# Optimization experiments

Hardware: AMD Instinct MI355X
Metric: run time of the kernel (lower is better)

## Reference

```python
import jax, jax.numpy as jnp
import numpy as np
from jax import lax

IN_CH = 256
OUT_CH = 256
INTER = IN_CH // 2
KERNEL = 3


def setup_inputs() -> dict:
    key = jax.random.key(0)
    ks = jax.random.split(key, 6)
    B, C, H, W = 8, IN_CH, 128, 128
    x = jax.random.normal(ks[0], (B, C, H, W), dtype=jnp.float32)
    s = 1.0 / np.sqrt(C)
    Wq = jax.random.normal(ks[1], (INTER, C), dtype=jnp.float32) * s
    Wk = jax.random.normal(ks[2], (INTER, C), dtype=jnp.float32) * s
    Wv = jax.random.normal(ks[3], (INTER, C), dtype=jnp.float32) * s
    w1d = jax.random.normal(ks[4], (KERNEL,), dtype=jnp.float32) * (1.0 / np.sqrt(KERNEL))
    Wc = jax.random.normal(ks[5], (OUT_CH, INTER, 3, 3), dtype=jnp.float32) * (1.0 / np.sqrt(INTER * 9))
    return {"x": x, "Wq": Wq, "Wk": Wk, "Wv": Wv, "w1d": w1d, "Wc": Wc}


def reference(x, Wq, Wk, Wv, w1d, Wc):
    B, C, H, W = x.shape
    inter = Wq.shape[0]
    Hs, Ws = H // 4, W // 4  # 1x1 conv, stride 4, pad 0 == spatial subsample
    xs = x[:, :, ::4, ::4]  # [B, C, Hs, Ws]
    q = jnp.einsum('oc,bchw->bohw', Wq, xs).reshape(B, inter, Hs * Ws)  # [B, inter, N]
    k = jnp.einsum('oc,bchw->bohw', Wk, xs).reshape(B, inter, Hs * Ws)
    v = jnp.einsum('oc,bchw->bohw', Wv, xs).reshape(B, inter, Hs * Ws)
    # gate = softmax(Q^T K) over last dim, shape [B, N, N]
    scores = jnp.einsum('bcn,bcm->bnm', q, k)
    gate = jax.nn.softmax(scores, axis=-1)
    # gated value: [B, inter, N] -> [B, inter, Hs, Ws]
    gv = jnp.einsum('bnm,bcm->bcn', gate, v).reshape(B, inter, Hs, Ws)
    # ECA channel gating: global avg pool -> conv1d over channel dim -> sigmoid
    ca = gv.mean(axis=(2, 3))  # [B, inter]
    ca = lax.conv_general_dilated(
        ca[:, None, :],                     # [B, 1, inter]
        w1d[None, None, :],                 # [1, 1, K]
        window_strides=(1,), padding=[((KERNEL - 1) // 2,) * 2],
        dimension_numbers=('NCH', 'OIH', 'NCH'))
    ca = jax.nn.sigmoid(ca)[:, 0, :, None, None]  # [B, inter, 1, 1]
    out = gv * ca
    out = lax.conv_general_dilated(
        out, Wc, window_strides=(1, 1), padding='SAME',
        dimension_numbers=('NCHW', 'OIHW', 'NCHW'))
    return out, gate, ca
```

## Files before the change

### kernel.cpp

```cpp
#include <hip/hip_runtime.h>
#include <math.h>

#define B_   8
#define C_   256
#define CI_  128
#define N_   1024
#define HW_  32
#define CO_  256

typedef __bf16 v8bf __attribute__((ext_vector_type(8)));
typedef float  f32x4 __attribute__((ext_vector_type(4)));
typedef unsigned short ushort_t;

__device__ __forceinline__ unsigned short f2bf_rne(float f) {
    unsigned int u = __float_as_uint(f);
    unsigned int r = u + 0x7FFF + ((u >> 16) & 1);
    return (unsigned short)(r >> 16);
}
__device__ __forceinline__ float bf2f(unsigned short h) {
    return __uint_as_float(((unsigned int)h) << 16);
}
__device__ __forceinline__ v8bf ld8(const ushort_t* p) {
    return *(const v8bf*)p;
}

__global__ __launch_bounds__(256) void prep_w_kernel(
    const float* __restrict__ Wc,
    const float* __restrict__ Wq, const float* __restrict__ Wk,
    const float* __restrict__ Wv,
    ushort_t* __restrict__ Whi, ushort_t* __restrict__ Wlo,
    ushort_t* __restrict__ Wp_hi, ushort_t* __restrict__ Wp_lo)
{
    if (blockIdx.x < 1152) {
        int idx = blockIdx.x * 256 + threadIdx.x;
        int o = idx / 1152;
        int r = idx - o * 1152;
        int ci = r / 9;
        int tap = r - ci * 9;
        float v = Wc[idx];
        unsigned short h = f2bf_rne(v);
        unsigned short l = f2bf_rne(v - bf2f(h));
        int didx = o * 1152 + tap * 128 + ci;
        Whi[didx] = h; Wlo[didx] = l;
    } else {
        int j = (blockIdx.x - 1152) * 256 + threadIdx.x;
        int o = j >> 8, c = j & 255;
        float v = (o < 128) ? Wq[o * 256 + c]
                : (o < 256) ? Wk[(o - 128) * 256 + c]
                            : Wv[(o - 256) * 256 + c];
        unsigned short h = f2bf_rne(v);
        unsigned short l = f2bf_rne(v - bf2f(h));
        Wp_hi[j] = h; Wp_lo[j] = l;
    }
}

__global__ __launch_bounds__(256) void prep_x_kernel(
    const float* __restrict__ x,
    ushort_t* __restrict__ xs_hi, ushort_t* __restrict__ xs_lo)
{
    __shared__ ushort_t lh[32 * 264];
    __shared__ ushort_t ll[32 * 264];
    const int h = blockIdx.x, b = blockIdx.y;
    const int tid = threadIdx.x;
    const int w = tid & 31, cg = tid >> 5;
    for (int c0 = 0; c0 < 256; c0 += 8) {
        int c = c0 + cg;
        float v = x[((size_t)(b * C_ + c) * 128 + h * 4) * 128 + w * 4];
        unsigned short hi = f2bf_rne(v);
        unsigned short lo = f2bf_rne(v - bf2f(hi));
        lh[w * 264 + c] = hi;
        ll[w * 264 + c] = lo;
    }
    __syncthreads();
    const int ww = tid >> 3, cs = tid & 7;
    size_t dst = ((size_t)(b * N_) + h * 32 + ww) * 256 + cs * 32;
    #pragma unroll
    for (int t = 0; t < 4; ++t) {
        *(uint4*)&xs_hi[dst + t * 8] = *(uint4*)&lh[ww * 264 + cs * 32 + t * 8];
        *(uint4*)&xs_lo[dst + t * 8] = *(uint4*)&ll[ww * 264 + cs * 32 + t * 8];
    }
}

__global__ __launch_bounds__(256) void proj_mfma_kernel(
    const ushort_t* __restrict__ Wp_hi, const ushort_t* __restrict__ Wp_lo,
    const ushort_t* __restrict__ xs_hi, const ushort_t* __restrict__ xs_lo,
    ushort_t* __restrict__ qt_hi, ushort_t* __restrict__ qt_lo,
    ushort_t* __restrict__ kt_hi, ushort_t* __restrict__ kt_lo,
    ushort_t* __restrict__ vB_hi, ushort_t* __restrict__ vB_lo)
{
    const int n0 = blockIdx.x * 64;
    const int o0 = blockIdx.y * 64;
    const int b  = blockIdx.z;
    const int tid = threadIdx.x;
    const int l = tid & 63, wv = tid >> 6;
    const int wy = wv >> 1, wx = wv & 1;
    const int ln = l & 15, quad = l >> 4;

    f32x4 acc[2][2];
    #pragma unroll
    for (int i = 0; i < 2; ++i)
        #pragma unroll
        for (int j = 0; j < 2; ++j) acc[i][j] = (f32x4){0.f,0.f,0.f,0.f};

    const ushort_t* Ah_p[2]; const ushort_t* Al_p[2];
    const ushort_t* Bh_p[2]; const ushort_t* Bl_p[2];
    #pragma unroll
    for (int i = 0; i < 2; ++i) {
        size_t off = (size_t)(o0 + wy * 32 + i * 16 + ln) * 256 + quad * 8;
        Ah_p[i] = Wp_hi + off; Al_p[i] = Wp_lo + off;
    }
    #pragma unroll
    for (int j = 0; j < 2; ++j) {
        size_t off = ((size_t)(b * N_) + n0 + wx * 32 + j * 16 + ln) * 256 + quad * 8;
        Bh_p[j] = xs_hi + off; Bl_p[j] = xs_lo + off;
    }

    #pragma unroll 4
    for (int k0 = 0; k0 < 256; k0 += 32) {
        v8bf Ah[2], Al[2], Bh[2], Bl[2];
        #pragma unroll
        for (int i = 0; i < 2; ++i) { Ah[i] = ld8(Ah_p[i] + k0); Al[i] = ld8(Al_p[i] + k0); }
        #pragma unroll
        for (int j = 0; j < 2; ++j) { Bh[j] = ld8(Bh_p[j] + k0); Bl[j] = ld8(Bl_p[j] + k0); }
        #pragma unroll
        for (int i = 0; i < 2; ++i)
            #pragma unroll
            for (int j = 0; j < 2; ++j) {
                acc[i][j] = __builtin_amdgcn_mfma_f32_16x16x32_bf16(Ah[i], Bh[j], acc[i][j], 0, 0, 0);
                acc[i][j] = __builtin_amdgcn_mfma_f32_16x16x32_bf16(Ah[i], Bl[j], acc[i][j], 0, 0, 0);
                acc[i][j] = __builtin_amdgcn_mfma_f32_16x16x32_bf16(Al[i], Bh[j], acc[i][j], 0, 0, 0);
            }
    }

    if (o0 < 256) {
        ushort_t* th = (o0 < 128) ? qt_hi : kt_hi;
        ushort_t* tl = (o0 < 128) ? qt_lo : kt_lo;
        const int ob = o0 & 127;
        #pragma unroll
        for (int i = 0; i < 2; ++i)
            #pragma unroll
            for (int j = 0; j < 2; ++j) {
                int oo = ob + wy * 32 + i * 16 + quad * 4;
                int n  = n0 + wx * 32 + j * 16 + ln;
                unsigned int h01 = 0, h23 = 0, l01 = 0, l23 = 0;
                #pragma unroll
                for (int r = 0; r < 4; ++r) {
                    float f = acc[i][j][r];
                    unsigned short hh = f2bf_rne(f);
                    unsigned short lo = f2bf_rne(f - bf2f(hh));
                    if (r < 2) { h01 |= ((unsigned)hh) << (16 * r); l01 |= ((unsigned)lo) << (16 * r); }
                    else       { h23 |= ((unsigned)hh) << (16 * (r - 2)); l23 |= ((unsigned)lo) << (16 * (r - 2)); }
                }
                size_t off = ((size_t)(b * N_) + n) * 128 + oo;
                *(uint2*)&th[off] = make_uint2(h01, h23);
                *(uint2*)&tl[off] = make_uint2(l01, l23);
            }
    } else {
        #pragma unroll
        for (int i = 0; i < 2; ++i)
            #pragma unroll
            for (int j = 0; j < 2; ++j)
                #pragma unroll
                for (int r = 0; r < 4; ++r) {
                    int c = (o0 - 256) + wy * 32 + i * 16 + quad * 4 + r;
                    int m = n0 + wx * 32 + j * 16 + ln;
                    float f = acc[i][j][r];
                    unsigned short hh = f2bf_rne(f);
                    unsigned short lo = f2bf_rne(f - bf2f(hh));
                    size_t off = (((size_t)b * 32 + (m >> 5)) * 128 + c) * 32 + (m & 31);
                    vB_hi[off] = hh; vB_lo[off] = lo;
                }
    }
}

__global__ __launch_bounds__(256, 1) void attn_fused_kernel(
    const ushort_t* __restrict__ qt_hi, const ushort_t* __restrict__ qt_lo,
    const ushort_t* __restrict__ kt_hi, const ushort_t* __restrict__ kt_lo,
    const ushort_t* __restrict__ vB_hi, const ushort_t* __restrict__ vB_lo,
    float* __restrict__ gate, float* __restrict__ gv)
{
    __shared__ __align__(16) char gsm[65536];
    __shared__ float redA[4][32];
    __shared__ float redB[4][32];

    const int n0 = blockIdx.x * 32;
    const int b  = blockIdx.y;
    const int tid = threadIdx.x;
    const int l = tid & 63, w = tid >> 6;
    const int ln = l & 15, quad = l >> 4;
    const int Mw = w * 256;

    const ushort_t* qb_h = qt_hi + ((size_t)(b * N_) + n0) * 128;
    const ushort_t* qb_l = qt_lo + ((size_t)(b * N_) + n0) * 128;
    const ushort_t* kb_h = kt_hi + (size_t)(b * N_) * 128;
    const ushort_t* kb_l = kt_lo + (size_t)(b * N_) * 128;

    f32x4 acc[2][16];
    #pragma unroll
    for (int nt = 0; nt < 2; ++nt)
        #pragma unroll
        for (int mt = 0; mt < 16; ++mt) acc[nt][mt] = (f32x4){0.f,0.f,0.f,0.f};

    #pragma unroll
    for (int c0 = 0; c0 < 128; c0 += 32) {
        v8bf Ah[2], Al[2];
        #pragma unroll
        for (int nt = 0; nt < 2; ++nt) {
            size_t aoff = (size_t)(nt * 16 + ln) * 128 + c0 + quad * 8;
            Ah[nt] = ld8(qb_h + aoff); Al[nt] = ld8(qb_l + aoff);
        }
        #pragma unroll
        for (int mt = 0; mt < 16; ++mt) {
            size_t boff = (size_t)(Mw + mt * 16 + ln) * 128 + c0 + quad * 8;
            v8bf Bh = ld8(kb_h + boff);
            v8bf Bl = ld8(kb_l + boff);
            #pragma unroll
            for (int nt = 0; nt < 2; ++nt) {
                acc[nt][mt] = __builtin_amdgcn_mfma_f32_16x16x32_bf16(Ah[nt], Bh, acc[nt][mt], 0, 0, 0);
                acc[nt][mt] = __builtin_amdgcn_mfma_f32_16x16x32_bf16(Ah[nt], Bl, acc[nt][mt], 0, 0, 0);
                acc[nt][mt] = __builtin_amdgcn_mfma_f32_16x16x32_bf16(Al[nt], Bh, acc[nt][mt], 0, 0, 0);
            }
        }
    }

    float rmax[2][4];
    #pragma unroll
    for (int nt = 0; nt < 2; ++nt)
        #pragma unroll
        for (int r = 0; r < 4; ++r) {
            float m = acc[nt][0][r];
            #pragma unroll
            for (int mt = 1; mt < 16; ++mt) m = fmaxf(m, acc[nt][mt][r]);
            rmax[nt][r] = m;
        }
    #pragma unroll
    for (int nt = 0; nt < 2; ++nt)
        #pragma unroll
        for (int r = 0; r < 4; ++r) {
            float m = rmax[nt][r];
            #pragma unroll
            for (int xm = 1; xm <= 8; xm <<= 1) m = fmaxf(m, __shfl_xor(m, xm, 64));
            rmax[nt][r] = m;
        }
    if (ln == 0) {
        #pragma unroll
        for (int nt = 0; nt < 2; ++nt)
            #pragma unroll
            for (int r = 0; r < 4; ++r)
                redA[w][nt * 16 + quad * 4 + r] = rmax[nt][r];
    }
    __syncthreads();
    #pragma unroll
    for (int nt = 0; nt < 2; ++nt)
        #pragma unroll
        for (int r = 0; r < 4; ++r) {
            int row = nt * 16 + quad * 4 + r;
            rmax[nt][r] = fmaxf(fmaxf(redA[0][row], redA[1][row]),
                                fmaxf(redA[2][row], redA[3][row]));
        }

    float rsum[2][4];
    #pragma unroll
    for (int nt = 0; nt < 2; ++nt)
        #pragma unroll
        for (int r = 0; r < 4; ++r) {
            float s = 0.f;
            #pragma unroll
            for (int mt = 0; mt < 16; ++mt) {
                float e = __expf(acc[nt][mt][r] - rmax[nt][r]);
                acc[nt][mt][r] = e;
                s += e;
            }
            rsum[nt][r] = s;
        }
    #pragma unroll
    for (int nt = 0; nt < 2; ++nt)
        #pragma unroll
        for (int r = 0; r < 4; ++r) {
            float s = rsum[nt][r];
            #pragma unroll
            for (int xm = 1; xm <= 8; xm <<= 1) s += __shfl_xor(s, xm, 64);
            rsum[nt][r] = s;
        }
    if (ln == 0) {
        #pragma unroll
        for (int nt = 0; nt < 2; ++nt)
            #pragma unroll
            for (int r = 0; r < 4; ++r)
                redB[w][nt * 16 + quad * 4 + r] = rsum[nt][r];
    }
    __syncthreads();
    #pragma unroll
    for (int nt = 0; nt < 2; ++nt)
        #pragma unroll
        for (int r = 0; r < 4; ++r) {
            int row = nt * 16 + quad * 4 + r;
            float inv = 1.0f / (redB[0][row] + redB[1][row] + redB[2][row] + redB[3][row]);
            #pragma unroll
            for (int mt = 0; mt < 16; ++mt) acc[nt][mt][r] *= inv;
        }

    float* grow = gate + (size_t)b * N_ * N_;
    #pragma unroll
    for (int nt = 0; nt < 2; ++nt)
        #pragma unroll
        for (int r = 0; r < 4; ++r) {
            int n  = n0 + nt * 16 + quad * 4 + r;
            int nl = nt * 16 + quad * 4 + r;
            #pragma unroll
            for (int mt = 0; mt < 16; ++mt) {
                int m = Mw + mt * 16 + ln;
                float v = acc[nt][mt][r];
                grow[(size_t)n * N_ + m] = v;
                int chunk = m >> 3;
                int addr = nl * 2048 + (((chunk ^ (nl & 7))) << 4) + ((m & 7) << 1);
                *(ushort_t*)&gsm[addr] = f2bf_rne(v);
            }
        }
    __syncthreads();

    const ushort_t* vb_h = vB_hi + (size_t)b * CI_ * N_;
    const ushort_t* vb_l = vB_lo + (size_t)b * CI_ * N_;

    f32x4 acc2[2][2];
    #pragma unroll
    for (int ct = 0; ct < 2; ++ct)
        #pragma unroll
        for (int nt = 0; nt < 2; ++nt) acc2[ct][nt] = (f32x4){0.f,0.f,0.f,0.f};

    #pragma unroll 4
    for (int m0 = 0; m0 < 1024; m0 += 32) {
        v8bf Bg[2];
        #pragma unroll
        for (int nt = 0; nt < 2; ++nt) {
            int nl = nt * 16 + ln;
            int chunk = (m0 >> 3) + quad;
            Bg[nt] = *(const v8bf*)&gsm[nl * 2048 + (((chunk ^ (nl & 7))) << 4)];
        }
        #pragma unroll
        for (int ct = 0; ct < 2; ++ct) {
            int c = w * 32 + ct * 16 + ln;
            size_t aoff = (((size_t)(m0 >> 5)) * 128 + c) * 32 + quad * 8;
            v8bf Avh = ld8(vb_h + aoff);
            v8bf Avl = ld8(vb_l + aoff);
            #pragma unroll
            for (int nt = 0; nt < 2; ++nt) {
                acc2[ct][nt] = __builtin_amdgcn_mfma_f32_16x16x32_bf16(Avh, Bg[nt], acc2[ct][nt], 0, 0, 0);
                acc2[ct][nt] = __builtin_amdgcn_mfma_f32_16x16x32_bf16(Avl, Bg[nt], acc2[ct][nt], 0, 0, 0);
            }
        }
    }

    #pragma unroll
    for (int ct = 0; ct < 2; ++ct)
        #pragma unroll
        for (int nt = 0; nt < 2; ++nt)
            #pragma unroll
            for (int r = 0; r < 4; ++r) {
                int c = w * 32 + ct * 16 + quad * 4 + r;
                int n = n0 + nt * 16 + ln;
                gv[(size_t)(b * CI_ + c) * N_ + n] = acc2[ct][nt][r];
            }
}

__global__ __launch_bounds__(256) void mean_kernel(
    const float* __restrict__ gv, float* __restrict__ meanb)
{
    const int i = blockIdx.x, b = blockIdx.y;
    const int tid = threadIdx.x;
    const int wid = tid >> 6, lane = tid & 63;
    __shared__ float red[4];
    const float* base = gv + (size_t)(b * CI_ + i) * N_;
    float4 v = ((const float4*)base)[tid];
    float s = v.x + v.y + v.z + v.w;
    #pragma unroll
    for (int off = 32; off; off >>= 1) s += __shfl_xor(s, off, 64);
    if (lane == 0) red[wid] = s;
    __syncthreads();
    if (tid == 0)
        meanb[b * CI_ + i] = (red[0] + red[1] + red[2] + red[3]) * (1.0f / 1024.0f);
}

__global__ __launch_bounds__(1024) void ca_kernel(
    const float* __restrict__ meanb, const float* __restrict__ w1d,
    float* __restrict__ ca)
{
    const int t = threadIdx.x;
    const int i = t & 127;
    float left  = (i > 0)   ? meanb[t - 1] : 0.0f;
    float mid   = meanb[t];
    float right = (i < 127) ? meanb[t + 1] : 0.0f;
    float val = w1d[0] * left + w1d[1] * mid + w1d[2] * right;
    ca[t] = 1.0f / (1.0f + __expf(-val));
}

#define BHI 0
#define BLO 17408
#define AHI 34816
#define ALO 43008
__global__ __launch_bounds__(256) void conv_mfma_kernel(
    const float* __restrict__ gv, const float* __restrict__ ca,
    const ushort_t* __restrict__ Whi, const ushort_t* __restrict__ Wlo,
    float* __restrict__ out)
{
    __shared__ char smem[51200];
    const int b   = blockIdx.z;
    const int h0  = blockIdx.y * 2;
    const int o0  = blockIdx.x * 64;
    const int tid = threadIdx.x;
    const int l   = tid & 63;
    const int wv  = tid >> 6;
    const int wy  = wv >> 1;
    const int wx  = wv & 1;
    const int ln  = l & 15;
    const int quad = l >> 4;

    f32x4 acc[2][2];
    #pragma unroll
    for (int i = 0; i < 2; ++i)
        #pragma unroll
        for (int j = 0; j < 2; ++j)
            acc[i][j] = (f32x4){0.f, 0.f, 0.f, 0.f};

    for (int half = 0; half < 2; ++half) {
        __syncthreads();
        for (int u = tid; u < 136 * 16; u += 256) {
            int p   = u >> 4;
            int ciq = u & 15;
            int hrel = p / 34;
            int c    = p - hrel * 34;
            int gr = h0 + hrel - 1;
            int gc = c - 1;
            bool ok = ((unsigned)gr < 32u) && ((unsigned)gc < 32u);
            int cib = half * 64 + ciq * 4;
            unsigned int hx = 0, hy = 0, lx = 0, ly = 0;
            #pragma unroll
            for (int t = 0; t < 4; ++t) {
                float v = 0.0f;
                if (ok)
                    v = gv[(size_t)(b * CI_ + cib + t) * N_ + gr * 32 + gc]
                        * ca[b * CI_ + cib + t];
                unsigned short h = f2bf_rne(v);
                unsigned short lo = f2bf_rne(v - bf2f(h));
                if (t < 2) { hx |= ((unsigned)h) << (16 * t); lx |= ((unsigned)lo) << (16 * t); }
                else       { hy |= ((unsigned)h) << (16 * (t - 2)); ly |= ((unsigned)lo) << (16 * (t - 2)); }
            }
            int addr = p * 128 + (((ciq >> 1) ^ (p & 7)) << 4) + ((ciq & 1) << 3);
            *(uint2*)&smem[BHI + addr] = make_uint2(hx, hy);
            *(uint2*)&smem[BLO + addr] = make_uint2(lx, ly);
        }
        for (int tap = 0; tap < 9; ++tap) {
            __syncthreads();
            #pragma unroll
            for (int it = 0; it < 2; ++it) {
                int row = it * 32 + (tid >> 3);
                int s   = tid & 7;
                int csrc = s ^ (row & 7);
                size_t gsrc = (size_t)(o0 + row) * 1152 + tap * 128 + half * 64 + csrc * 8;
                int la = row * 128 + s * 16;
                *(uint4*)&smem[AHI + la] = *(const uint4*)&Whi[gsrc];
                *(uint4*)&smem[ALO + la] = *(const uint4*)&Wlo[gsrc];
            }
            __syncthreads();
            const int dy = tap / 3, dx = tap - dy * 3;
            const int pbase = (wx + dy) * 34 + dx;
            #pragma unroll
            for (int cc = 0; cc < 2; ++cc) {
                v8bf Bh[2], Bl[2], Ah[2], Al[2];
                #pragma unroll
                for (int j = 0; j < 2; ++j) {
                    int p = pbase + j * 16 + ln;
                    int ch = cc * 4 + quad;
                    int addr = p * 128 + ((ch ^ (p & 7)) << 4);
                    Bh[j] = *(const v8bf*)&smem[BHI + addr];
                    Bl[j] = *(const v8bf*)&smem[BLO + addr];
                }
                #pragma unroll
                for (int i = 0; i < 2; ++i) {
                    int o = wy * 32 + i * 16 + ln;
                    int ch = cc * 4 + quad;
                    int addr = o * 128 + ((ch ^ (o & 7)) << 4);
                    Ah[i] = *(const v8bf*)&smem[AHI + addr];
                    Al[i] = *(const v8bf*)&smem[ALO + addr];
                }
                #pragma unroll
                for (int i = 0; i < 2; ++i)
                    #pragma unroll
                    for (int j = 0; j < 2; ++j) {
                        acc[i][j] = __builtin_amdgcn_mfma_f32_16x16x32_bf16(Ah[i], Bh[j], acc[i][j], 0, 0, 0);
                        acc[i][j] = __builtin_amdgcn_mfma_f32_16x16x32_bf16(Ah[i], Bl[j], acc[i][j], 0, 0, 0);
                        acc[i][j] = __builtin_amdgcn_mfma_f32_16x16x32_bf16(Al[i], Bh[j], acc[i][j], 0, 0, 0);
                    }
            }
        }
    }

    const int h = h0 + wx;
    #pragma unroll
    for (int i = 0; i < 2; ++i)
        #pragma unroll
        for (int j = 0; j < 2; ++j)
            #pragma unroll
            for (int r = 0; r < 4; ++r) {
                int o = o0 + wy * 32 + i * 16 + quad * 4 + r;
                int w = j * 16 + ln;
                out[(size_t)(b * CO_ + o) * N_ + h * 32 + w] = acc[i][j][r];
            }
}

extern "C" void kernel_launch(void* const* d_in, const int* in_sizes, int n_in,
                              void* d_out, int out_size, void* d_ws, size_t ws_size,
                              hipStream_t stream) {
    const float* x   = (const float*)d_in[0];
    const float* Wq  = (const float*)d_in[1];
    const float* Wk  = (const float*)d_in[2];
    const float* Wv  = (const float*)d_in[3];
    const float* w1d = (const float*)d_in[4];
    const float* Wc  = (const float*)d_in[5];

    float* out  = (float*)d_out;
    float* gate = out + 2097152;
    float* ca   = gate + 8388608;

    float*    gv      = (float*)d_ws;
    float*    meanb   = gv + 1048576;
    ushort_t* Whi     = (ushort_t*)(meanb + 1024);
    ushort_t* Wlo     = Whi + 294912;
    ushort_t* Wp_hi   = Wlo + 294912;
    ushort_t* Wp_lo   = Wp_hi + 98304;
    ushort_t* xs_hi   = Wp_lo + 98304;
    ushort_t* xs_lo   = xs_hi + 2097152;
    ushort_t* qt_hi   = xs_lo + 2097152;
    ushort_t* qt_lo   = qt_hi + 1048576;
    ushort_t* kt_hi   = qt_lo + 1048576;
    ushort_t* kt_lo   = kt_hi + 1048576;
    ushort_t* vB_hi   = kt_lo + 1048576;
    ushort_t* vB_lo   = vB_hi + 1048576;

    prep_w_kernel<<<dim3(1536), 256, 0, stream>>>(Wc, Wq, Wk, Wv, Whi, Wlo, Wp_hi, Wp_lo);
    prep_x_kernel<<<dim3(32, 8), 256, 0, stream>>>(x, xs_hi, xs_lo);
    proj_mfma_kernel<<<dim3(16, 6, 8), 256, 0, stream>>>(
        Wp_hi, Wp_lo, xs_hi, xs_lo, qt_hi, qt_lo, kt_hi, kt_lo, vB_hi, vB_lo);
    attn_fused_kernel<<<dim3(32, 8), 256, 0, stream>>>(
        qt_hi, qt_lo, kt_hi, kt_lo, vB_hi, vB_lo, gate, gv);
    mean_kernel<<<dim3(128, 8), 256, 0, stream>>>(gv, meanb);
    ca_kernel<<<1, 1024, 0, stream>>>(meanb, w1d, ca);
    conv_mfma_kernel<<<dim3(4, 16, 8), 256, 0, stream>>>(gv, ca, Whi, Wlo, out);
}
```

Measured before the change: 307.1 us.

## Fuse prep kernels, widen attention to 512 threads, fold mean into attention, prefetch conv weights

Merges the weight and input prep kernels into one launch and batches the x loads into registers. The attention kernel now runs 8 waves per block with half the key columns each. It writes gv channel-last and accumulates the channel means by atomics, which removes the separate mean kernel. The conv kernel reads gv as float4 in the new layout and double-buffers the per-tap weight tiles in shared memory, prefetching the next tap while computing the current one. The cost is atomic float accumulation, which makes summation order nondeterministic, plus more shared memory in the conv kernel.

```diff
diff --git a/kernel.cpp b/kernel.cpp
--- a/kernel.cpp
+++ b/kernel.cpp
@@ -24,15 +24,26 @@
     return *(const v8bf*)p;
 }
 
-__global__ __launch_bounds__(256) void prep_w_kernel(
+__global__ __launch_bounds__(256) void prep_all_kernel(
+    const float* __restrict__ x,
     const float* __restrict__ Wc,
     const float* __restrict__ Wq, const float* __restrict__ Wk,
     const float* __restrict__ Wv,
     ushort_t* __restrict__ Whi, ushort_t* __restrict__ Wlo,
-    ushort_t* __restrict__ Wp_hi, ushort_t* __restrict__ Wp_lo)
+    ushort_t* __restrict__ Wp_hi, ushort_t* __restrict__ Wp_lo,
+    ushort_t* __restrict__ xs_hi, ushort_t* __restrict__ xs_lo,
+    float* __restrict__ meanb)
 {
-    if (blockIdx.x < 1152) {
-        int idx = blockIdx.x * 256 + threadIdx.x;
+    __shared__ ushort_t lh[32 * 264];
+    __shared__ ushort_t ll[32 * 264];
+    const int bx = blockIdx.x;
+    const int tid = threadIdx.x;
+
+    if (bx < 1152) {
+        if (bx == 0) {
+            *(float4*)&meanb[tid * 4] = make_float4(0.f, 0.f, 0.f, 0.f);
+        }
+        int idx = bx * 256 + tid;
         int o = idx / 1152;
         int r = idx - o * 1152;
         int ci = r / 9;
@@ -42,8 +53,8 @@
         unsigned short l = f2bf_rne(v - bf2f(h));
         int didx = o * 1152 + tap * 128 + ci;
         Whi[didx] = h; Wlo[didx] = l;
-    } else {
-        int j = (blockIdx.x - 1152) * 256 + threadIdx.x;
+    } else if (bx < 1536) {
+        int j = (bx - 1152) * 256 + tid;
         int o = j >> 8, c = j & 255;
         float v = (o < 128) ? Wq[o * 256 + c]
                 : (o < 256) ? Wk[(o - 128) * 256 + c]
@@ -51,33 +62,32 @@
         unsigned short h = f2bf_rne(v);
         unsigned short l = f2bf_rne(v - bf2f(h));
         Wp_hi[j] = h; Wp_lo[j] = l;
-    }
-}
-
-__global__ __launch_bounds__(256) void prep_x_kernel(
-    const float* __restrict__ x,
-    ushort_t* __restrict__ xs_hi, ushort_t* __restrict__ xs_lo)
-{
-    __shared__ ushort_t lh[32 * 264];
-    __shared__ ushort_t ll[32 * 264];
-    const int h = blockIdx.x, b = blockIdx.y;
-    const int tid = threadIdx.x;
-    const int w = tid & 31, cg = tid >> 5;
-    for (int c0 = 0; c0 < 256; c0 += 8) {
-        int c = c0 + cg;
-        float v = x[((size_t)(b * C_ + c) * 128 + h * 4) * 128 + w * 4];
-        unsigned short hi = f2bf_rne(v);
-        unsigned short lo = f2bf_rne(v - bf2f(hi));
-        lh[w * 264 + c] = hi;
-        ll[w * 264 + c] = lo;
-    }
-    __syncthreads();
-    const int ww = tid >> 3, cs = tid & 7;
-    size_t dst = ((size_t)(b * N_) + h * 32 + ww) * 256 + cs * 32;
-    #pragma unroll
-    for (int t = 0; t < 4; ++t) {
-        *(uint4*)&xs_hi[dst + t * 8] = *(uint4*)&lh[ww * 264 + cs * 32 + t * 8];
-        *(uint4*)&xs_lo[dst + t * 8] = *(uint4*)&ll[ww * 264 + cs * 32 + t * 8];
+    } else {
+        const int bx2 = bx - 1536;
+        const int h = bx2 & 31, b = bx2 >> 5;
+        const int w = tid & 31, cg = tid >> 5;
+        float v[32];
+        #pragma unroll
+        for (int i = 0; i < 32; ++i) {
+            int c = i * 8 + cg;
+            v[i] = x[((size_t)(b * C_ + c) * 128 + h * 4) * 128 + w * 4];
+        }
+        #pragma unroll
+        for (int i = 0; i < 32; ++i) {
+            int c = i * 8 + cg;
+            unsigned short hi = f2bf_rne(v[i]);
+            unsigned short lo = f2bf_rne(v[i] - bf2f(hi));
+            lh[w * 264 + c] = hi;
+            ll[w * 264 + c] = lo;
+        }
+        __syncthreads();
+        const int ww = tid >> 3, cs = tid & 7;
+        size_t dst = ((size_t)(b * N_) + h * 32 + ww) * 256 + cs * 32;
+        #pragma unroll
+        for (int t = 0; t < 4; ++t) {
+            *(uint4*)&xs_hi[dst + t * 8] = *(uint4*)&lh[ww * 264 + cs * 32 + t * 8];
+            *(uint4*)&xs_lo[dst + t * 8] = *(uint4*)&ll[ww * 264 + cs * 32 + t * 8];
+        }
     }
 }
 
@@ -173,33 +183,33 @@
     }
 }
 
-__global__ __launch_bounds__(256, 1) void attn_fused_kernel(
+__global__ __launch_bounds__(512, 2) void attn_fused_kernel(
     const ushort_t* __restrict__ qt_hi, const ushort_t* __restrict__ qt_lo,
     const ushort_t* __restrict__ kt_hi, const ushort_t* __restrict__ kt_lo,
     const ushort_t* __restrict__ vB_hi, const ushort_t* __restrict__ vB_lo,
-    float* __restrict__ gate, float* __restrict__ gv)
+    float* __restrict__ gate, float* __restrict__ gv, float* __restrict__ meanb)
 {
     __shared__ __align__(16) char gsm[65536];
-    __shared__ float redA[4][32];
-    __shared__ float redB[4][32];
+    __shared__ float redA[8][32];
+    __shared__ float redB[8][32];
 
     const int n0 = blockIdx.x * 32;
     const int b  = blockIdx.y;
     const int tid = threadIdx.x;
     const int l = tid & 63, w = tid >> 6;
     const int ln = l & 15, quad = l >> 4;
-    const int Mw = w * 256;
+    const int Mw = w * 128;
 
     const ushort_t* qb_h = qt_hi + ((size_t)(b * N_) + n0) * 128;
     const ushort_t* qb_l = qt_lo + ((size_t)(b * N_) + n0) * 128;
     const ushort_t* kb_h = kt_hi + (size_t)(b * N_) * 128;
     const ushort_t* kb_l = kt_lo + (size_t)(b * N_) * 128;
 
-    f32x4 acc[2][16];
-    #pragma unroll
-    for (int nt = 0; nt < 2; ++nt)
-        #pragma unroll
-        for (int mt = 0; mt < 16; ++mt) acc[nt][mt] = (f32x4){0.f,0.f,0.f,0.f};
+    f32x4 acc[2][8];
+    #pragma unroll
+    for (int nt = 0; nt < 2; ++nt)
+        #pragma unroll
+        for (int mt = 0; mt < 8; ++mt) acc[nt][mt] = (f32x4){0.f,0.f,0.f,0.f};
 
     #pragma unroll
     for (int c0 = 0; c0 < 128; c0 += 32) {
@@ -210,7 +220,7 @@
             Ah[nt] = ld8(qb_h + aoff); Al[nt] = ld8(qb_l + aoff);
         }
         #pragma unroll
-        for (int mt = 0; mt < 16; ++mt) {
+        for (int mt = 0; mt < 8; ++mt) {
             size_t boff = (size_t)(Mw + mt * 16 + ln) * 128 + c0 + quad * 8;
             v8bf Bh = ld8(kb_h + boff);
             v8bf Bl = ld8(kb_l + boff);
@@ -230,7 +240,7 @@
         for (int r = 0; r < 4; ++r) {
             float m = acc[nt][0][r];
             #pragma unroll
-            for (int mt = 1; mt < 16; ++mt) m = fmaxf(m, acc[nt][mt][r]);
+            for (int mt = 1; mt < 8; ++mt) m = fmaxf(m, acc[nt][mt][r]);
             rmax[nt][r] = m;
         }
     #pragma unroll
@@ -255,8 +265,11 @@
         #pragma unroll
         for (int r = 0; r < 4; ++r) {
             int row = nt * 16 + quad * 4 + r;
-            rmax[nt][r] = fmaxf(fmaxf(redA[0][row], redA[1][row]),
-                                fmaxf(redA[2][row], redA[3][row]));
+            float m0 = fmaxf(fmaxf(redA[0][row], redA[1][row]),
+                             fmaxf(redA[2][row], redA[3][row]));
+            float m1 = fmaxf(fmaxf(redA[4][row], redA[5][row]),
+                             fmaxf(redA[6][row], redA[7][row]));
+            rmax[nt][r] = fmaxf(m0, m1);
         }
 
     float rsum[2][4];
@@ -266,7 +279,7 @@
         for (int r = 0; r < 4; ++r) {
             float s = 0.f;
             #pragma unroll
-            for (int mt = 0; mt < 16; ++mt) {
+            for (int mt = 0; mt < 8; ++mt) {
                 float e = __expf(acc[nt][mt][r] - rmax[nt][r]);
                 acc[nt][mt][r] = e;
                 s += e;
@@ -295,9 +308,10 @@
         #pragma unroll
         for (int r = 0; r < 4; ++r) {
             int row = nt * 16 + quad * 4 + r;
-            float inv = 1.0f / (redB[0][row] + redB[1][row] + redB[2][row] + redB[3][row]);
-            #pragma unroll
-            for (int mt = 0; mt < 16; ++mt) acc[nt][mt][r] *= inv;
+            float inv = 1.0f / ((redB[0][row] + redB[1][row] + redB[2][row] + redB[3][row]) +
+                                (redB[4][row] + redB[5][row] + redB[6][row] + redB[7][row]));
+            #pragma unroll
+            for (int mt = 0; mt < 8; ++mt) acc[nt][mt][r] *= inv;
         }
 
     float* grow = gate + (size_t)b * N_ * N_;
@@ -308,7 +322,7 @@
             int n  = n0 + nt * 16 + quad * 4 + r;
             int nl = nt * 16 + quad * 4 + r;
             #pragma unroll
-            for (int mt = 0; mt < 16; ++mt) {
+            for (int mt = 0; mt < 8; ++mt) {
                 int m = Mw + mt * 16 + ln;
                 float v = acc[nt][mt][r];
                 grow[(size_t)n * N_ + m] = v;
@@ -322,11 +336,9 @@
     const ushort_t* vb_h = vB_hi + (size_t)b * CI_ * N_;
     const ushort_t* vb_l = vB_lo + (size_t)b * CI_ * N_;
 
-    f32x4 acc2[2][2];
-    #pragma unroll
-    for (int ct = 0; ct < 2; ++ct)
-        #pragma unroll
-        for (int nt = 0; nt < 2; ++nt) acc2[ct][nt] = (f32x4){0.f,0.f,0.f,0.f};
+    f32x4 acc2[2];
+    acc2[0] = (f32x4){0.f,0.f,0.f,0.f};
+    acc2[1] = (f32x4){0.f,0.f,0.f,0.f};
 
     #pragma unroll 4
     for (int m0 = 0; m0 < 1024; m0 += 32) {
@@ -337,48 +349,42 @@
             int chunk = (m0 >> 3) + quad;
             Bg[nt] = *(const v8bf*)&gsm[nl * 2048 + (((chunk ^ (nl & 7))) << 4)];
         }
-        #pragma unroll
-        for (int ct = 0; ct < 2; ++ct) {
-            int c = w * 32 + ct * 16 + ln;
-            size_t aoff = (((size_t)(m0 >> 5)) * 128 + c) * 32 + quad * 8;
-            v8bf Avh = ld8(vb_h + aoff);
-            v8bf Avl = ld8(vb_l + aoff);
-            #pragma unroll
-            for (int nt = 0; nt < 2; ++nt) {
-                acc2[ct][nt] = __builtin_amdgcn_mfma_f32_16x16x32_bf16(Avh, Bg[nt], acc2[ct][nt], 0, 0, 0);
-                acc2[ct][nt] = __builtin_amdgcn_mfma_f32_16x16x32_bf16(Avl, Bg[nt], acc2[ct][nt], 0, 0, 0);
-            }
-        }
-    }
-
-    #pragma unroll
-    for (int ct = 0; ct < 2; ++ct)
-        #pragma unroll
-        for (int nt = 0; nt < 2; ++nt)
-            #pragma unroll
-            for (int r = 0; r < 4; ++r) {
-                int c = w * 32 + ct * 16 + quad * 4 + r;
-                int n = n0 + nt * 16 + ln;
-                gv[(size_t)(b * CI_ + c) * N_ + n] = acc2[ct][nt][r];
-            }
-}
-
-__global__ __launch_bounds__(256) void mean_kernel(
-    const float* __restrict__ gv, float* __restrict__ meanb)
-{
-    const int i = blockIdx.x, b = blockIdx.y;
-    const int tid = threadIdx.x;
-    const int wid = tid >> 6, lane = tid & 63;
-    __shared__ float red[4];
-    const float* base = gv + (size_t)(b * CI_ + i) * N_;
-    float4 v = ((const float4*)base)[tid];
-    float s = v.x + v.y + v.z + v.w;
-    #pragma unroll
-    for (int off = 32; off; off >>= 1) s += __shfl_xor(s, off, 64);
-    if (lane == 0) red[wid] = s;
-    __syncthreads();
-    if (tid == 0)
-        meanb[b * CI_ + i] = (red[0] + red[1] + red[2] + red[3]) * (1.0f / 1024.0f);
+        int c = w * 16 + ln;
+        size_t aoff = (((size_t)(m0 >> 5)) * 128 + c) * 32 + quad * 8;
+        v8bf Avh = ld8(vb_h + aoff);
+        v8bf Avl = ld8(vb_l + aoff);
+        #pragma unroll
+        for (int nt = 0; nt < 2; ++nt) {
+            acc2[nt] = __builtin_amdgcn_mfma_f32_16x16x32_bf16(Avh, Bg[nt], acc2[nt], 0, 0, 0);
+            acc2[nt] = __builtin_amdgcn_mfma_f32_16x16x32_bf16(Avl, Bg[nt], acc2[nt], 0, 0, 0);
+        }
+    }
+
+    #pragma unroll
+    for (int nt = 0; nt < 2; ++nt) {
+        int n = n0 + nt * 16 + ln;
+        float4 o4 = make_float4(acc2[nt][0], acc2[nt][1], acc2[nt][2], acc2[nt][3]);
+        *(float4*)&gv[((size_t)(b * N_) + n) * CI_ + w * 16 + quad * 4] = o4;
+    }
+
+    float s0 = acc2[0][0] + acc2[1][0];
+    float s1 = acc2[0][1] + acc2[1][1];
+    float s2 = acc2[0][2] + acc2[1][2];
+    float s3 = acc2[0][3] + acc2[1][3];
+    #pragma unroll
+    for (int xm = 1; xm <= 8; xm <<= 1) {
+        s0 += __shfl_xor(s0, xm, 64);
+        s1 += __shfl_xor(s1, xm, 64);
+        s2 += __shfl_xor(s2, xm, 64);
+        s3 += __shfl_xor(s3, xm, 64);
+    }
+    if (ln == 0) {
+        int cb = b * CI_ + w * 16 + quad * 4;
+        atomicAdd(&meanb[cb + 0], s0);
+        atomicAdd(&meanb[cb + 1], s1);
+        atomicAdd(&meanb[cb + 2], s2);
+        atomicAdd(&meanb[cb + 3], s3);
+    }
 }
 
 __global__ __launch_bounds__(1024) void ca_kernel(
@@ -387,23 +393,25 @@
 {
     const int t = threadIdx.x;
     const int i = t & 127;
-    float left  = (i > 0)   ? meanb[t - 1] : 0.0f;
-    float mid   = meanb[t];
-    float right = (i < 127) ? meanb[t + 1] : 0.0f;
+    const float sc = 1.0f / 1024.0f;
+    float left  = (i > 0)   ? meanb[t - 1] * sc : 0.0f;
+    float mid   = meanb[t] * sc;
+    float right = (i < 127) ? meanb[t + 1] * sc : 0.0f;
     float val = w1d[0] * left + w1d[1] * mid + w1d[2] * right;
     ca[t] = 1.0f / (1.0f + __expf(-val));
 }
 
-#define BHI 0
-#define BLO 17408
-#define AHI 34816
-#define ALO 43008
+#define BHI  0
+#define BLO  17408
 __global__ __launch_bounds__(256) void conv_mfma_kernel(
     const float* __restrict__ gv, const float* __restrict__ ca,
     const ushort_t* __restrict__ Whi, const ushort_t* __restrict__ Wlo,
     float* __restrict__ out)
 {
-    __shared__ char smem[51200];
+    __shared__ __align__(16) char smem[67584];
+    const int AH[2] = {34816, 51200};
+    const int AL[2] = {43008, 59392};
+
     const int b   = blockIdx.z;
     const int h0  = blockIdx.y * 2;
     const int o0  = blockIdx.x * 64;
@@ -421,6 +429,10 @@
         #pragma unroll
         for (int j = 0; j < 2; ++j)
             acc[i][j] = (f32x4){0.f, 0.f, 0.f, 0.f};
+
+    const int srow0 = tid >> 3, scol = tid & 7;
+    const int la0 = srow0 * 128 + scol * 16;
+    const int la1 = (srow0 + 32) * 128 + scol * 16;
 
     for (int half = 0; half < 2; ++half) {
         __syncthreads();
@@ -433,15 +445,18 @@
             int gc = c - 1;
             bool ok = ((unsigned)gr < 32u) && ((unsigned)gc < 32u);
             int cib = half * 64 + ciq * 4;
+            float vv[4] = {0.f, 0.f, 0.f, 0.f};
+            if (ok) {
+                float4 v4 = *(const float4*)&gv[((size_t)(b * N_) + gr * 32 + gc) * CI_ + cib];
+                float4 c4 = *(const float4*)&ca[b * CI_ + cib];
+                vv[0] = v4.x * c4.x; vv[1] = v4.y * c4.y;
+                vv[2] = v4.z * c4.z; vv[3] = v4.w * c4.w;
+            }
             unsigned int hx = 0, hy = 0, lx = 0, ly = 0;
             #pragma unroll
             for (int t = 0; t < 4; ++t) {
-                float v = 0.0f;
-                if (ok)
-                    v = gv[(size_t)(b * CI_ + cib + t) * N_ + gr * 32 + gc]
-                        * ca[b * CI_ + cib + t];
-                unsigned short h = f2bf_rne(v);
-                unsigned short lo = f2bf_rne(v - bf2f(h));
+                unsigned short h = f2bf_rne(vv[t]);
+                unsigned short lo = f2bf_rne(vv[t] - bf2f(h));
                 if (t < 2) { hx |= ((unsigned)h) << (16 * t); lx |= ((unsigned)lo) << (16 * t); }
                 else       { hy |= ((unsigned)h) << (16 * (t - 2)); ly |= ((unsigned)lo) << (16 * (t - 2)); }
             }
@@ -449,24 +464,41 @@
             *(uint2*)&smem[BHI + addr] = make_uint2(hx, hy);
             *(uint2*)&smem[BLO + addr] = make_uint2(lx, ly);
         }
+        {
+            int csrc0 = scol ^ (srow0 & 7);
+            int csrc1 = scol ^ ((srow0 + 32) & 7);
+            size_t g0 = (size_t)(o0 + srow0) * 1152 + half * 64 + csrc0 * 8;
+            size_t g1 = (size_t)(o0 + srow0 + 32) * 1152 + half * 64 + csrc1 * 8;
+            uint4 h0r = *(const uint4*)&Whi[g0];
+            uint4 l0r = *(const uint4*)&Wlo[g0];
+            uint4 h1r = *(const uint4*)&Whi[g1];
+            uint4 l1r = *(const uint4*)&Wlo[g1];
+            *(uint4*)&smem[AH[0] + la0] = h0r;
+            *(uint4*)&smem[AL[0] + la0] = l0r;
+            *(uint4*)&smem[AH[0] + la1] = h1r;
+            *(uint4*)&smem[AL[0] + la1] = l1r;
+        }
+
         for (int tap = 0; tap < 9; ++tap) {
             __syncthreads();
-            #pragma unroll
-            for (int it = 0; it < 2; ++it) {
-                int row = it * 32 + (tid >> 3);
-                int s   = tid & 7;
-                int csrc = s ^ (row & 7);
-                size_t gsrc = (size_t)(o0 + row) * 1152 + tap * 128 + half * 64 + csrc * 8;
-                int la = row * 128 + s * 16;
-                *(uint4*)&smem[AHI + la] = *(const uint4*)&Whi[gsrc];
-                *(uint4*)&smem[ALO + la] = *(const uint4*)&Wlo[gsrc];
-            }
-            __syncthreads();
+            uint4 nh0, nl0, nh1, nl1;
+            if (tap < 8) {
+                int ntap = tap + 1;
+                int csrc0 = scol ^ (srow0 & 7);
+                int csrc1 = scol ^ ((srow0 + 32) & 7);
+                size_t g0 = (size_t)(o0 + srow0) * 1152 + ntap * 128 + half * 64 + csrc0 * 8;
+                size_t g1 = (size_t)(o0 + srow0 + 32) * 1152 + ntap * 128 + half * 64 + csrc1 * 8;
+                nh0 = *(const uint4*)&Whi[g0];
+                nl0 = *(const uint4*)&Wlo[g0];
+                nh1 = *(const uint4*)&Whi[g1];
+                nl1 = *(const uint4*)&Wlo[g1];
+            }
+            const int ah = AH[tap & 1], al = AL[tap & 1];
             const int dy = tap / 3, dx = tap - dy * 3;
             const int pbase = (wx + dy) * 34 + dx;
             #pragma unroll
             for (int cc = 0; cc < 2; ++cc) {
-                v8bf Bh[2], Bl[2], Ah[2], Al[2];
+                v8bf Bh[2], Bl[2], Ah2[2], Al2[2];
                 #pragma unroll
                 for (int j = 0; j < 2; ++j) {
                     int p = pbase + j * 16 + ln;
@@ -480,17 +512,24 @@
                     int o = wy * 32 + i * 16 + ln;
                     int ch = cc * 4 + quad;
                     int addr = o * 128 + ((ch ^ (o & 7)) << 4);
-                    Ah[i] = *(const v8bf*)&smem[AHI + addr];
-                    Al[i] = *(const v8bf*)&smem[ALO + addr];
+                    Ah2[i] = *(const v8bf*)&smem[ah + addr];
+                    Al2[i] = *(const v8bf*)&smem[al + addr];
                 }
                 #pragma unroll
                 for (int i = 0; i < 2; ++i)
                     #pragma unroll
                     for (int j = 0; j < 2; ++j) {
-                        acc[i][j] = __builtin_amdgcn_mfma_f32_16x16x32_bf16(Ah[i], Bh[j], acc[i][j], 0, 0, 0);
-                        acc[i][j] = __builtin_amdgcn_mfma_f32_16x16x32_bf16(Ah[i], Bl[j], acc[i][j], 0, 0, 0);
-                        acc[i][j] = __builtin_amdgcn_mfma_f32_16x16x32_bf16(Al[i], Bh[j], acc[i][j], 0, 0, 0);
+                        acc[i][j] = __builtin_amdgcn_mfma_f32_16x16x32_bf16(Ah2[i], Bh[j], acc[i][j], 0, 0, 0);
+                        acc[i][j] = __builtin_amdgcn_mfma_f32_16x16x32_bf16(Ah2[i], Bl[j], acc[i][j], 0, 0, 0);
+                        acc[i][j] = __builtin_amdgcn_mfma_f32_16x16x32_bf16(Al2[i], Bh[j], acc[i][j], 0, 0, 0);
                     }
+            }
+            if (tap < 8) {
+                int nb = (tap + 1) & 1;
+                *(uint4*)&smem[AH[nb] + la0] = nh0;
+                *(uint4*)&smem[AL[nb] + la0] = nl0;
+                *(uint4*)&smem[AH[nb] + la1] = nh1;
+                *(uint4*)&smem[AL[nb] + la1] = nl1;
             }
         }
     }
@@ -537,13 +576,12 @@
     ushort_t* vB_hi   = kt_lo + 1048576;
     ushort_t* vB_lo   = vB_hi + 1048576;
 
-    prep_w_kernel<<<dim3(1536), 256, 0, stream>>>(Wc, Wq, Wk, Wv, Whi, Wlo, Wp_hi, Wp_lo);
-    prep_x_kernel<<<dim3(32, 8), 256, 0, stream>>>(x, xs_hi, xs_lo);
+    prep_all_kernel<<<dim3(1792), 256, 0, stream>>>(
+        x, Wc, Wq, Wk, Wv, Whi, Wlo, Wp_hi, Wp_lo, xs_hi, xs_lo, meanb);
     proj_mfma_kernel<<<dim3(16, 6, 8), 256, 0, stream>>>(
         Wp_hi, Wp_lo, xs_hi, xs_lo, qt_hi, qt_lo, kt_hi, kt_lo, vB_hi, vB_lo);
-    attn_fused_kernel<<<dim3(32, 8), 256, 0, stream>>>(
-        qt_hi, qt_lo, kt_hi, kt_lo, vB_hi, vB_lo, gate, gv);
-    mean_kernel<<<dim3(128, 8), 256, 0, stream>>>(gv, meanb);
+    attn_fused_kernel<<<dim3(32, 8), 512, 0, stream>>>(
+        qt_hi, qt_lo, kt_hi, kt_lo, vB_hi, vB_lo, gate, gv, meanb);
     ca_kernel<<<1, 1024, 0, stream>>>(meanb, w1d, ca);
     conv_mfma_kernel<<<dim3(4, 16, 8), 256, 0, stream>>>(gv, ca, Whi, Wlo, out);
 }
```

Result: faster. 286.8 us (-6.6%).
